# Optimization experiments

Hardware: AMD Instinct MI355X
Metric: run time of the kernel (lower is better)

The kernel has to match this reference:

```python
import jax, jax.numpy as jnp
import numpy as np

B, F, T, C, H, HH = 16384, 2048, 64, 32, 24, 48  # batch, features, n_tails, cluster_size, tail_hidden, head_hidden


def setup_inputs() -> dict:
    key = jax.random.key(0)
    ks = jax.random.split(key, 8)
    x = jax.random.normal(ks[0], (B, F), dtype=jnp.float32)
    clusters = jnp.arange(T * C, dtype=jnp.int32).reshape(T, C)  # equal-size partition of features
    # tied autoencoder weights: encoder = x @ W + hb, decoder = h @ W.T + vb
    Wt = jax.random.normal(ks[1], (T, C, H), dtype=jnp.float32) * 0.1
    hb = jax.random.normal(ks[2], (T, H), dtype=jnp.float32) * 0.1
    vb = jax.random.normal(ks[3], (T, C), dtype=jnp.float32) * 0.1
    Wh = jax.random.normal(ks[4], (T, HH), dtype=jnp.float32) * 0.1
    hbh = jax.random.normal(ks[5], (HH,), dtype=jnp.float32) * 0.1
    vbh = jax.random.normal(ks[6], (T,), dtype=jnp.float32) * 0.1
    return {"x": x, "clusters": clusters, "Wt": Wt, "hb": hb, "vb": vb,
            "Wh": Wh, "hbh": hbh, "vbh": vbh}


def reference(x, clusters, Wt, hb, vb, Wh, hbh, vbh):
    # gather all clusters in one shot: [B, T, C]
    xg = x[:, clusters]
    # batched tiny autoencoders (encode then decode with tied weight W)
    h = jnp.einsum('btc,tch->bth', xg, Wt) + hb[None, :, :]
    out = jnp.einsum('bth,tch->btc', h, Wt) + vb[None, :, :]
    # per-tail log-RMSE over (batch, cluster) elements -> [T]
    rmse = jnp.sqrt(jnp.mean(jnp.square(out - xg), axis=(0, 2)))
    tails = jnp.log(rmse)
    # head autoencoder on the tail-loss vector
    hh = tails @ Wh + hbh          # [HH]
    head_out = hh @ Wh.T + vbh     # [T]
    return head_out, tails
```

## Files before the change

### kernel.cpp

```cpp
#include <hip/hip_runtime.h>
#include <cstddef>

#define B_   16384
#define F_   2048
#define T_   64
#define C_   32
#define H_   24
#define HH_  48
#define THR  256
#define TPB  8
#define RB   128
#define NCH  (B_ / RB)
#define NBLK ((T_ / TPB) * NCH)
#define XST  264
#define SLST 72
#define FRAG_F 2048
#define OF_BW0 0
#define OF_BW1 1024
#define OF_GG0 2048
#define OF_GG1 3072
#define OF_DD  6144
#define OF_K0  6656
#define OF_W2  6912

typedef __attribute__((ext_vector_type(8))) short  short8;
typedef __attribute__((ext_vector_type(4))) float  floatx4;

__device__ __forceinline__ short f2bf(float f) {
    union { float f; unsigned u; } v; v.f = f;
    unsigned r = v.u + 0x7FFFu + ((v.u >> 16) & 1u);
    return (short)(r >> 16);
}

__global__ __launch_bounds__(64) void kitnet_prep(
    const float* __restrict__ Wt, const float* __restrict__ hb,
    const float* __restrict__ vb, float* __restrict__ frag)
{
    __shared__ float WL[C_ * H_];
    __shared__ float hbL[H_];
    __shared__ float w2L[C_];
    const int t = blockIdx.x, lane = threadIdx.x;

    for (int i = lane; i < C_ * H_; i += 64) WL[i] = Wt[t * C_ * H_ + i];
    if (lane < H_) hbL[lane] = hb[t * H_ + lane];
    __syncthreads();
    if (lane < C_) {
        float a = vb[t * C_ + lane];
        #pragma unroll
        for (int j = 0; j < H_; ++j) a += WL[lane * H_ + j] * hbL[j];
        w2L[lane] = a;
    }
    __syncthreads();

    const int m = lane & 15, q = lane >> 4;
    char* fb = (char*)(frag + (size_t)t * FRAG_F);

    short8 bw0, bw1, gg0, gg1;
    #pragma unroll
    for (int j = 0; j < 8; ++j) {
        const int k = q * 8 + j;
        bw0[j] = f2bf(WL[k * H_ + m]);
        bw1[j] = (m < 8) ? f2bf(WL[k * H_ + 16 + m]) : (short)0;
        float a0 = 0.f, a1 = 0.f;
        if (k < H_) {
            #pragma unroll
            for (int c = 0; c < C_; ++c) {
                a0 += WL[c * H_ + k] * WL[c * H_ + m];
                if (m < 8) a1 += WL[c * H_ + k] * WL[c * H_ + 16 + m];
            }
            if (k == m)      a0 -= 2.f;
            if (k == 16 + m) a1 -= 2.f;
        }
        gg0[j] = (k < H_) ? f2bf(a0) : (short)0;
        gg1[j] = (k < H_ && m < 8) ? f2bf(a1) : (short)0;
    }
    float dm0 = 0.f, dm1 = 0.f;
    #pragma unroll
    for (int c = 0; c < C_; ++c) {
        dm0 += w2L[c] * WL[c * H_ + m];
        if (m < 8) dm1 += w2L[c] * WL[c * H_ + 16 + m];
    }

    *(short8*)(fb + OF_BW0 + lane * 16) = bw0;
    *(short8*)(fb + OF_BW1 + lane * 16) = bw1;
    *(short8*)(fb + OF_GG0 + lane * 16) = gg0;
    *(short8*)(fb + OF_GG1 + lane * 16) = gg1;
    ((float*)(fb + OF_DD))[lane * 2]     = 2.f * dm0;
    ((float*)(fb + OF_DD))[lane * 2 + 1] = (m < 8) ? 2.f * dm1 : 0.f;
    if (lane < C_) ((float*)(fb + OF_W2))[lane] = w2L[lane];
    if (lane == 0) {
        float a = 0.f;
        #pragma unroll
        for (int c = 0; c < C_; ++c) a += w2L[c] * w2L[c];
        *(float*)(fb + OF_K0) = a;
    }
}

__global__ __launch_bounds__(THR) void kitnet_main(
    const float* __restrict__ x, const float* __restrict__ frag,
    float* __restrict__ partial)
{
    __shared__ __align__(16) short xb[2][16 * XST];
    __shared__ __align__(16) short Sl[8 * 16 * SLST];
    __shared__ float tsum[TPB];

    const int tid   = threadIdx.x;
    const int tg    = blockIdx.x & (T_ / TPB - 1);
    const int chunk = blockIdx.x >> 3;
    const int lane  = tid & 63, wid = tid >> 6;
    const int m = lane & 15, q = lane >> 4;
    const int lr = tid >> 4, ls = tid & 15;

    if (tid < TPB) tsum[tid] = 0.f;

    const char* fb0 = (const char*)frag + (size_t)(tg * TPB + 2 * wid) * (FRAG_F * 4);
    const char* fb1 = fb0 + (FRAG_F * 4);
    const short8 bw0a = *(const short8*)(fb0 + OF_BW0 + lane * 16);
    const short8 bw1a = *(const short8*)(fb0 + OF_BW1 + lane * 16);
    const short8 gg0a = *(const short8*)(fb0 + OF_GG0 + lane * 16);
    const short8 gg1a = *(const short8*)(fb0 + OF_GG1 + lane * 16);
    const short8 bw0b = *(const short8*)(fb1 + OF_BW0 + lane * 16);
    const short8 bw1b = *(const short8*)(fb1 + OF_BW1 + lane * 16);
    const short8 gg0b = *(const short8*)(fb1 + OF_GG0 + lane * 16);
    const short8 gg1b = *(const short8*)(fb1 + OF_GG1 + lane * 16);
    const float* ddp0 = (const float*)(fb0 + OF_DD) + lane * 2;
    const float* ddp1 = (const float*)(fb1 + OF_DD) + lane * 2;
    const float d0a = ddp0[0], d1a = ddp0[1];
    const float d0b = ddp1[0], d1b = ddp1[1];

    const float* w2p = (const float*)((const char*)frag
        + (size_t)(tg * TPB + (ls >> 1)) * (FRAG_F * 4) + OF_W2) + (ls & 1) * 16;
    const float4 w2v0 = *(const float4*)(w2p);
    const float4 w2v1 = *(const float4*)(w2p + 4);
    const float4 w2v2 = *(const float4*)(w2p + 8);
    const float4 w2v3 = *(const float4*)(w2p + 12);
    const float* xsrc = x + (size_t)(chunk * RB + lr) * F_ + tg * (TPB * C_) + ls * 16;

    float xs = 0.f, err_a = 0.f, err_b = 0.f;
    short* sla = &Sl[(wid * 2 + 0) * 16 * SLST];
    short* slb = &Sl[(wid * 2 + 1) * 16 * SLST];
    short* xb0 = &xb[0][0];
    short* xb1 = &xb[1][0];

#define STORE(XBP)                                                            \
    {                                                                         \
        xs += v0.x * (v0.x - 2.f * w2v0.x) + v0.y * (v0.y - 2.f * w2v0.y)     \
            + v0.z * (v0.z - 2.f * w2v0.z) + v0.w * (v0.w - 2.f * w2v0.w)     \
            + v1.x * (v1.x - 2.f * w2v1.x) + v1.y * (v1.y - 2.f * w2v1.y)     \
            + v1.z * (v1.z - 2.f * w2v1.z) + v1.w * (v1.w - 2.f * w2v1.w)     \
            + v2.x * (v2.x - 2.f * w2v2.x) + v2.y * (v2.y - 2.f * w2v2.y)     \
            + v2.z * (v2.z - 2.f * w2v2.z) + v2.w * (v2.w - 2.f * w2v2.w)     \
            + v3.x * (v3.x - 2.f * w2v3.x) + v3.y * (v3.y - 2.f * w2v3.y)     \
            + v3.z * (v3.z - 2.f * w2v3.z) + v3.w * (v3.w - 2.f * w2v3.w);    \
        short8 lo8 = { f2bf(v0.x), f2bf(v0.y), f2bf(v0.z), f2bf(v0.w),        \
                       f2bf(v1.x), f2bf(v1.y), f2bf(v1.z), f2bf(v1.w) };      \
        short8 hi8 = { f2bf(v2.x), f2bf(v2.y), f2bf(v2.z), f2bf(v2.w),        \
                       f2bf(v3.x), f2bf(v3.y), f2bf(v3.z), f2bf(v3.w) };      \
        short* wp = (XBP) + lr * XST + ls * 16;                               \
        *(short8*)wp = lo8;                                                   \
        *(short8*)(wp + 8) = hi8;                                             \
    }

#define COMPUTE(XBP)                                                          \
    {                                                                         \
        const short* xp = (XBP) + m * XST + wid * (2 * C_) + q * 8;           \
        short8 sfa = *(const short8*)(xp);                                    \
        short8 sfb = *(const short8*)(xp + C_);                               \
        const floatx4 z_ = {0.f, 0.f, 0.f, 0.f};                              \
        floatx4 S0a = __builtin_amdgcn_mfma_f32_16x16x32_bf16(sfa, bw0a, z_, 0, 0, 0); \
        floatx4 S1a = __builtin_amdgcn_mfma_f32_16x16x32_bf16(sfa, bw1a, z_, 0, 0, 0); \
        floatx4 S0b = __builtin_amdgcn_mfma_f32_16x16x32_bf16(sfb, bw0b, z_, 0, 0, 0); \
        floatx4 S1b = __builtin_amdgcn_mfma_f32_16x16x32_bf16(sfb, bw1b, z_, 0, 0, 0); \
        _Pragma("unroll")                                                     \
        for (int r = 0; r < 4; ++r) {                                         \
            sla[(q * 4 + r) * SLST + m]      = f2bf(S0a[r]);                  \
            sla[(q * 4 + r) * SLST + 16 + m] = f2bf(S1a[r]);                  \
            slb[(q * 4 + r) * SLST + m]      = f2bf(S0b[r]);                  \
            slb[(q * 4 + r) * SLST + 16 + m] = f2bf(S1b[r]);                  \
        }                                                                     \
        short8 pfa = *(const short8*)&sla[m * SLST + q * 8];                  \
        short8 pfb = *(const short8*)&slb[m * SLST + q * 8];                  \
        floatx4 Q0a = __builtin_amdgcn_mfma_f32_16x16x32_bf16(pfa, gg0a, z_, 0, 0, 0); \
        floatx4 Q1a = __builtin_amdgcn_mfma_f32_16x16x32_bf16(pfa, gg1a, z_, 0, 0, 0); \
        floatx4 Q0b = __builtin_amdgcn_mfma_f32_16x16x32_bf16(pfb, gg0b, z_, 0, 0, 0); \
        floatx4 Q1b = __builtin_amdgcn_mfma_f32_16x16x32_bf16(pfb, gg1b, z_, 0, 0, 0); \
        _Pragma("unroll")                                                     \
        for (int r = 0; r < 4; ++r) {                                         \
            err_a += (Q0a[r] + d0a) * S0a[r] + (Q1a[r] + d1a) * S1a[r];       \
            err_b += (Q0b[r] + d0b) * S0b[r] + (Q1b[r] + d1b) * S1b[r];       \
        }                                                                     \
    }

    float4 v0 = *(const float4*)(xsrc);
    float4 v1 = *(const float4*)(xsrc + 4);
    float4 v2 = *(const float4*)(xsrc + 8);
    float4 v3 = *(const float4*)(xsrc + 12);
    STORE(xb0);
    __syncthreads();

    #pragma unroll 2
    for (int g = 0; g < 8; ++g) {
        short* cur = (g & 1) ? xb1 : xb0;
        short* nxt = (g & 1) ? xb0 : xb1;
        if (g < 7) {
            const float* s = xsrc + (size_t)(g + 1) * (16 * F_);
            v0 = *(const float4*)(s);
            v1 = *(const float4*)(s + 4);
            v2 = *(const float4*)(s + 8);
            v3 = *(const float4*)(s + 12);
        }
        COMPUTE(cur);
        if (g < 7) {
            STORE(nxt);
            __syncthreads();
        }
    }
#undef STORE
#undef COMPUTE

    #pragma unroll
    for (int off = 32; off > 0; off >>= 1) {
        err_a += __shfl_down(err_a, off, 64);
        err_b += __shfl_down(err_b, off, 64);
    }
    if (lane == 0) {
        atomicAdd(&tsum[wid * 2],     err_a);
        atomicAdd(&tsum[wid * 2 + 1], err_b);
    }
    xs += __shfl_down(xs, 32, 64);
    xs += __shfl_down(xs, 16, 64);
    xs += __shfl_down(xs, 1, 64);
    if (lane < 16 && !(lane & 1)) atomicAdd(&tsum[lane >> 1], xs);
    __syncthreads();
    if (tid < TPB)
        partial[(size_t)(tg * TPB + tid) * NCH + chunk] = tsum[tid];
}

__global__ __launch_bounds__(64) void kitnet_head(
    const float* __restrict__ partial, const float* __restrict__ frag,
    const float* __restrict__ Wh, const float* __restrict__ hbh,
    const float* __restrict__ vbh, float* __restrict__ out)
{
    __shared__ float tl[T_];
    __shared__ float hhL[HH_];
    const int tid = threadIdx.x;

    float sse = (float)B_ *
        *(const float*)((const char*)frag + (size_t)tid * (FRAG_F * 4) + OF_K0);
    const float4* p = (const float4*)(partial + (size_t)tid * NCH);
    #pragma unroll 8
    for (int i = 0; i < NCH / 4; ++i) {
        float4 t4 = p[i];
        sse += t4.x + t4.y + t4.z + t4.w;
    }

    const float tail = 0.5f * logf(sse * (1.0f / ((float)B_ * (float)C_)));
    tl[tid] = tail;
    out[T_ + tid] = tail;
    __syncthreads();

    if (tid < HH_) {
        float acc = hbh[tid];
        #pragma unroll 8
        for (int t = 0; t < T_; ++t) acc += tl[t] * Wh[t * HH_ + tid];
        hhL[tid] = acc;
    }
    __syncthreads();

    float ho = vbh[tid];
    #pragma unroll 8
    for (int j = 0; j < HH_; ++j) ho += hhL[j] * Wh[tid * HH_ + j];
    out[tid] = ho;
}

extern "C" void kernel_launch(void* const* d_in, const int* in_sizes, int n_in,
                              void* d_out, int out_size, void* d_ws, size_t ws_size,
                              hipStream_t stream)
{
    const float* x        = (const float*)d_in[0];
    const int*   clusters = (const int*)  d_in[1];  (void)clusters;
    const float* Wt       = (const float*)d_in[2];
    const float* hb       = (const float*)d_in[3];
    const float* vb       = (const float*)d_in[4];
    const float* Wh       = (const float*)d_in[5];
    const float* hbh      = (const float*)d_in[6];
    const float* vbh      = (const float*)d_in[7];
    float* out  = (float*)d_out;
    float* frag    = (float*)d_ws;
    float* partial = (float*)d_ws + (size_t)T_ * FRAG_F;

    kitnet_prep<<<dim3(T_), dim3(64), 0, stream>>>(Wt, hb, vb, frag);
    kitnet_main<<<dim3(NBLK), dim3(THR), 0, stream>>>(x, frag, partial);
    kitnet_head<<<dim3(1), dim3(64), 0, stream>>>(partial, frag, Wh, hbh, vbh, out);
}
```

Measured before the change: 229.9 us.

## Restructure main kernel to sweep all tails per 16-row block

Each block now owns 16 batch rows and walks all 2048 features in 256-wide column chunks, instead of owning 8 tails and 128 rows. Rows are read as contiguous full-width strips, which is meant to improve DRAM locality. Weight fragments are reloaded from global memory for each chunk and partial sums are written per block for all 64 tails. The head kernel reduces the larger 1024x64 partial array with 256 threads, at the cost of more fragment reloads and a bigger final reduction.

```diff
diff --git a/kernel.cpp b/kernel.cpp
--- a/kernel.cpp
+++ b/kernel.cpp
@@ -8,10 +8,10 @@
 #define H_   24
 #define HH_  48
 #define THR  256
-#define TPB  8
-#define RB   128
-#define NCH  (B_ / RB)
-#define NBLK ((T_ / TPB) * NCH)
+#define RPB  16
+#define NBLK (B_ / RPB)
+#define CW   256
+#define NCC  (F_ / CW)
 #define XST  264
 #define SLST 72
 #define FRAG_F 2048
@@ -34,7 +34,8 @@
 
 __global__ __launch_bounds__(64) void kitnet_prep(
     const float* __restrict__ Wt, const float* __restrict__ hb,
-    const float* __restrict__ vb, float* __restrict__ frag)
+    const float* __restrict__ vb, float* __restrict__ frag,
+    float* __restrict__ w2d)
 {
     __shared__ float WL[C_ * H_];
     __shared__ float hbL[H_];
@@ -49,6 +50,7 @@
         #pragma unroll
         for (int j = 0; j < H_; ++j) a += WL[lane * H_ + j] * hbL[j];
         w2L[lane] = a;
+        w2d[t * C_ + lane] = a;
     }
     __syncthreads();
 
@@ -87,7 +89,6 @@
     *(short8*)(fb + OF_GG1 + lane * 16) = gg1;
     ((float*)(fb + OF_DD))[lane * 2]     = 2.f * dm0;
     ((float*)(fb + OF_DD))[lane * 2 + 1] = (m < 8) ? 2.f * dm1 : 0.f;
-    if (lane < C_) ((float*)(fb + OF_W2))[lane] = w2L[lane];
     if (lane == 0) {
         float a = 0.f;
         #pragma unroll
@@ -96,69 +97,44 @@
     }
 }
 
-__global__ __launch_bounds__(THR) void kitnet_main(
+__global__ __launch_bounds__(THR, 4) void kitnet_main(
     const float* __restrict__ x, const float* __restrict__ frag,
-    float* __restrict__ partial)
-{
-    __shared__ __align__(16) short xb[2][16 * XST];
+    const float* __restrict__ w2d, float* __restrict__ partial)
+{
+    __shared__ __align__(16) short xb0s[RPB * XST];
+    __shared__ __align__(16) short xb1s[RPB * XST];
     __shared__ __align__(16) short Sl[8 * 16 * SLST];
-    __shared__ float tsum[TPB];
-
-    const int tid   = threadIdx.x;
-    const int tg    = blockIdx.x & (T_ / TPB - 1);
-    const int chunk = blockIdx.x >> 3;
-    const int lane  = tid & 63, wid = tid >> 6;
+    __shared__ float tsumL[T_];
+
+    const int tid  = threadIdx.x;
+    const int bid  = blockIdx.x;
+    const int lane = tid & 63, wid = tid >> 6;
     const int m = lane & 15, q = lane >> 4;
-    const int lr = tid >> 4, ls = tid & 15;
-
-    if (tid < TPB) tsum[tid] = 0.f;
-
-    const char* fb0 = (const char*)frag + (size_t)(tg * TPB + 2 * wid) * (FRAG_F * 4);
-    const char* fb1 = fb0 + (FRAG_F * 4);
-    const short8 bw0a = *(const short8*)(fb0 + OF_BW0 + lane * 16);
-    const short8 bw1a = *(const short8*)(fb0 + OF_BW1 + lane * 16);
-    const short8 gg0a = *(const short8*)(fb0 + OF_GG0 + lane * 16);
-    const short8 gg1a = *(const short8*)(fb0 + OF_GG1 + lane * 16);
-    const short8 bw0b = *(const short8*)(fb1 + OF_BW0 + lane * 16);
-    const short8 bw1b = *(const short8*)(fb1 + OF_BW1 + lane * 16);
-    const short8 gg0b = *(const short8*)(fb1 + OF_GG0 + lane * 16);
-    const short8 gg1b = *(const short8*)(fb1 + OF_GG1 + lane * 16);
-    const float* ddp0 = (const float*)(fb0 + OF_DD) + lane * 2;
-    const float* ddp1 = (const float*)(fb1 + OF_DD) + lane * 2;
-    const float d0a = ddp0[0], d1a = ddp0[1];
-    const float d0b = ddp1[0], d1b = ddp1[1];
-
-    const float* w2p = (const float*)((const char*)frag
-        + (size_t)(tg * TPB + (ls >> 1)) * (FRAG_F * 4) + OF_W2) + (ls & 1) * 16;
-    const float4 w2v0 = *(const float4*)(w2p);
-    const float4 w2v1 = *(const float4*)(w2p + 4);
-    const float4 w2v2 = *(const float4*)(w2p + 8);
-    const float4 w2v3 = *(const float4*)(w2p + 12);
-    const float* xsrc = x + (size_t)(chunk * RB + lr) * F_ + tg * (TPB * C_) + ls * 16;
-
-    float xs = 0.f, err_a = 0.f, err_b = 0.f;
+    const int r0 = bid * RPB;
+
+    if (tid < T_) tsumL[tid] = 0.f;
+
+    const float* xwp = x + (size_t)(r0 + wid * 4) * F_ + lane * 4;
     short* sla = &Sl[(wid * 2 + 0) * 16 * SLST];
     short* slb = &Sl[(wid * 2 + 1) * 16 * SLST];
-    short* xb0 = &xb[0][0];
-    short* xb1 = &xb[1][0];
-
-#define STORE(XBP)                                                            \
+
+    float err_all = 0.f;
+
+#define PK(VV, K)                                                             \
+        xs += VV.x * (VV.x - 2.f * w2v.x) + VV.y * (VV.y - 2.f * w2v.y)       \
+            + VV.z * (VV.z - 2.f * w2v.z) + VV.w * (VV.w - 2.f * w2v.w);      \
+        { short4 p_ = { f2bf(VV.x), f2bf(VV.y), f2bf(VV.z), f2bf(VV.w) };     \
+          *(short4*)(wp_ + (K) * XST) = p_; }
+
+#define STORE(XBP, CIDX)                                                      \
     {                                                                         \
-        xs += v0.x * (v0.x - 2.f * w2v0.x) + v0.y * (v0.y - 2.f * w2v0.y)     \
-            + v0.z * (v0.z - 2.f * w2v0.z) + v0.w * (v0.w - 2.f * w2v0.w)     \
-            + v1.x * (v1.x - 2.f * w2v1.x) + v1.y * (v1.y - 2.f * w2v1.y)     \
-            + v1.z * (v1.z - 2.f * w2v1.z) + v1.w * (v1.w - 2.f * w2v1.w)     \
-            + v2.x * (v2.x - 2.f * w2v2.x) + v2.y * (v2.y - 2.f * w2v2.y)     \
-            + v2.z * (v2.z - 2.f * w2v2.z) + v2.w * (v2.w - 2.f * w2v2.w)     \
-            + v3.x * (v3.x - 2.f * w2v3.x) + v3.y * (v3.y - 2.f * w2v3.y)     \
-            + v3.z * (v3.z - 2.f * w2v3.z) + v3.w * (v3.w - 2.f * w2v3.w);    \
-        short8 lo8 = { f2bf(v0.x), f2bf(v0.y), f2bf(v0.z), f2bf(v0.w),        \
-                       f2bf(v1.x), f2bf(v1.y), f2bf(v1.z), f2bf(v1.w) };      \
-        short8 hi8 = { f2bf(v2.x), f2bf(v2.y), f2bf(v2.z), f2bf(v2.w),        \
-                       f2bf(v3.x), f2bf(v3.y), f2bf(v3.z), f2bf(v3.w) };      \
-        short* wp = (XBP) + lr * XST + ls * 16;                               \
-        *(short8*)wp = lo8;                                                   \
-        *(short8*)(wp + 8) = hi8;                                             \
+        float xs = 0.f;                                                       \
+        short* wp_ = (XBP) + (wid * 4) * XST + lane * 4;                      \
+        PK(v0, 0) PK(v1, 1) PK(v2, 2) PK(v3, 3)                               \
+        xs += __shfl_xor(xs, 1, 64);                                          \
+        xs += __shfl_xor(xs, 2, 64);                                          \
+        xs += __shfl_xor(xs, 4, 64);                                          \
+        if ((lane & 7) == 0) atomicAdd(&tsumL[(CIDX) * 8 + (lane >> 3)], xs); \
     }
 
 #define COMPUTE(XBP)                                                          \
@@ -191,86 +167,111 @@
         }                                                                     \
     }
 
-    float4 v0 = *(const float4*)(xsrc);
-    float4 v1 = *(const float4*)(xsrc + 4);
-    float4 v2 = *(const float4*)(xsrc + 8);
-    float4 v3 = *(const float4*)(xsrc + 12);
-    STORE(xb0);
-    __syncthreads();
-
-    #pragma unroll 2
-    for (int g = 0; g < 8; ++g) {
-        short* cur = (g & 1) ? xb1 : xb0;
-        short* nxt = (g & 1) ? xb0 : xb1;
-        if (g < 7) {
-            const float* s = xsrc + (size_t)(g + 1) * (16 * F_);
-            v0 = *(const float4*)(s);
-            v1 = *(const float4*)(s + 4);
-            v2 = *(const float4*)(s + 8);
-            v3 = *(const float4*)(s + 12);
-        }
-        COMPUTE(cur);
-        if (g < 7) {
-            STORE(nxt);
+    float4 v0 = *(const float4*)(xwp + 0 * F_);
+    float4 v1 = *(const float4*)(xwp + 1 * F_);
+    float4 v2 = *(const float4*)(xwp + 2 * F_);
+    float4 v3 = *(const float4*)(xwp + 3 * F_);
+    float4 w2v = *(const float4*)(w2d + lane * 4);
+    __syncthreads();
+    STORE(xb0s, 0)
+    __syncthreads();
+
+    for (int cc = 0; cc < NCC; ++cc) {
+        short* cur = (cc & 1) ? xb1s : xb0s;
+        short* nxt = (cc & 1) ? xb0s : xb1s;
+        if (cc < NCC - 1) {
+            const float* s = xwp + (size_t)(cc + 1) * CW;
+            v0 = *(const float4*)(s + 0 * F_);
+            v1 = *(const float4*)(s + 1 * F_);
+            v2 = *(const float4*)(s + 2 * F_);
+            v3 = *(const float4*)(s + 3 * F_);
+            w2v = *(const float4*)(w2d + (cc + 1) * CW + lane * 4);
+        }
+        const char* fbA = (const char*)frag
+            + (size_t)(cc * 8 + 2 * wid) * (FRAG_F * 4);
+        const char* fbB = fbA + (FRAG_F * 4);
+        const short8 bw0a = *(const short8*)(fbA + OF_BW0 + lane * 16);
+        const short8 bw1a = *(const short8*)(fbA + OF_BW1 + lane * 16);
+        const short8 gg0a = *(const short8*)(fbA + OF_GG0 + lane * 16);
+        const short8 gg1a = *(const short8*)(fbA + OF_GG1 + lane * 16);
+        const short8 bw0b = *(const short8*)(fbB + OF_BW0 + lane * 16);
+        const short8 bw1b = *(const short8*)(fbB + OF_BW1 + lane * 16);
+        const short8 gg0b = *(const short8*)(fbB + OF_GG0 + lane * 16);
+        const short8 gg1b = *(const short8*)(fbB + OF_GG1 + lane * 16);
+        const float2 dA = *(const float2*)(fbA + OF_DD + lane * 8);
+        const float2 dB = *(const float2*)(fbB + OF_DD + lane * 8);
+        const float d0a = dA.x, d1a = dA.y;
+        const float d0b = dB.x, d1b = dB.y;
+
+        float err_a = 0.f, err_b = 0.f;
+        COMPUTE(cur)
+
+        #pragma unroll
+        for (int off = 32; off > 0; off >>= 1) {
+            err_a += __shfl_down(err_a, off, 64);
+            err_b += __shfl_down(err_b, off, 64);
+        }
+        if (lane == 0) {
+            atomicAdd(&tsumL[cc * 8 + 2 * wid],     err_a);
+            atomicAdd(&tsumL[cc * 8 + 2 * wid + 1], err_b);
+        }
+        if (cc < NCC - 1) {
+            STORE(nxt, cc + 1)
             __syncthreads();
         }
     }
+#undef PK
 #undef STORE
 #undef COMPUTE
-
-    #pragma unroll
-    for (int off = 32; off > 0; off >>= 1) {
-        err_a += __shfl_down(err_a, off, 64);
-        err_b += __shfl_down(err_b, off, 64);
-    }
-    if (lane == 0) {
-        atomicAdd(&tsum[wid * 2],     err_a);
-        atomicAdd(&tsum[wid * 2 + 1], err_b);
-    }
-    xs += __shfl_down(xs, 32, 64);
-    xs += __shfl_down(xs, 16, 64);
-    xs += __shfl_down(xs, 1, 64);
-    if (lane < 16 && !(lane & 1)) atomicAdd(&tsum[lane >> 1], xs);
-    __syncthreads();
-    if (tid < TPB)
-        partial[(size_t)(tg * TPB + tid) * NCH + chunk] = tsum[tid];
-}
-
-__global__ __launch_bounds__(64) void kitnet_head(
+    (void)err_all;
+
+    __syncthreads();
+    if (tid < T_)
+        partial[(size_t)bid * T_ + tid] = tsumL[tid];
+}
+
+__global__ __launch_bounds__(256) void kitnet_head(
     const float* __restrict__ partial, const float* __restrict__ frag,
     const float* __restrict__ Wh, const float* __restrict__ hbh,
     const float* __restrict__ vbh, float* __restrict__ out)
 {
+    __shared__ float red[4][T_];
     __shared__ float tl[T_];
     __shared__ float hhL[HH_];
     const int tid = threadIdx.x;
-
-    float sse = (float)B_ *
-        *(const float*)((const char*)frag + (size_t)tid * (FRAG_F * 4) + OF_K0);
-    const float4* p = (const float4*)(partial + (size_t)tid * NCH);
-    #pragma unroll 8
-    for (int i = 0; i < NCH / 4; ++i) {
-        float4 t4 = p[i];
-        sse += t4.x + t4.y + t4.z + t4.w;
-    }
-
-    const float tail = 0.5f * logf(sse * (1.0f / ((float)B_ * (float)C_)));
-    tl[tid] = tail;
-    out[T_ + tid] = tail;
+    const int t = tid & 63, qq = tid >> 6;
+
+    float s = 0.f;
+    #pragma unroll 4
+    for (int b = qq * (NBLK / 4); b < (qq + 1) * (NBLK / 4); ++b)
+        s += partial[(size_t)b * T_ + t];
+    red[qq][t] = s;
+    __syncthreads();
+
+    if (tid < T_) {
+        float sse = red[0][tid] + red[1][tid] + red[2][tid] + red[3][tid]
+            + (float)B_ * *(const float*)((const char*)frag
+                  + (size_t)tid * (FRAG_F * 4) + OF_K0);
+        const float tail = 0.5f * logf(sse * (1.0f / ((float)B_ * (float)C_)));
+        tl[tid] = tail;
+        out[T_ + tid] = tail;
+    }
     __syncthreads();
 
     if (tid < HH_) {
         float acc = hbh[tid];
         #pragma unroll 8
-        for (int t = 0; t < T_; ++t) acc += tl[t] * Wh[t * HH_ + tid];
+        for (int t2 = 0; t2 < T_; ++t2) acc += tl[t2] * Wh[t2 * HH_ + tid];
         hhL[tid] = acc;
     }
     __syncthreads();
 
-    float ho = vbh[tid];
-    #pragma unroll 8
-    for (int j = 0; j < HH_; ++j) ho += hhL[j] * Wh[tid * HH_ + j];
-    out[tid] = ho;
+    if (tid < T_) {
+        float ho = vbh[tid];
+        #pragma unroll 8
+        for (int j = 0; j < HH_; ++j) ho += hhL[j] * Wh[tid * HH_ + j];
+        out[tid] = ho;
+    }
 }
 
 extern "C" void kernel_launch(void* const* d_in, const int* in_sizes, int n_in,
@@ -285,11 +286,13 @@
     const float* Wh       = (const float*)d_in[5];
     const float* hbh      = (const float*)d_in[6];
     const float* vbh      = (const float*)d_in[7];
-    float* out  = (float*)d_out;
+    float* out = (float*)d_out;
+
     float* frag    = (float*)d_ws;
-    float* partial = (float*)d_ws + (size_t)T_ * FRAG_F;
-
-    kitnet_prep<<<dim3(T_), dim3(64), 0, stream>>>(Wt, hb, vb, frag);
-    kitnet_main<<<dim3(NBLK), dim3(THR), 0, stream>>>(x, frag, partial);
-    kitnet_head<<<dim3(1), dim3(64), 0, stream>>>(partial, frag, Wh, hbh, vbh, out);
-}
+    float* w2d     = frag + (size_t)T_ * FRAG_F;
+    float* partial = w2d + T_ * C_;
+
+    kitnet_prep<<<dim3(T_), dim3(64), 0, stream>>>(Wt, hb, vb, frag, w2d);
+    kitnet_main<<<dim3(NBLK), dim3(THR), 0, stream>>>(x, frag, w2d, partial);
+    kitnet_head<<<dim3(1), dim3(256), 0, stream>>>(partial, frag, Wh, hbh, vbh, out);
+}
```

After: 241.9 us. 5.2% more time.
